# Kernel optimization log

Measured on AMD Instinct MI355X. Metric: run time of the kernel, lower is better.

The kernel has to match this reference:

```python
import jax, jax.numpy as jnp
import numpy as np

B, H, W, C = 32, 56, 56, 256
NH, WS, SH = 8, 7, 3
HD = C // NH
SCALE = HD ** -0.5
N = WS * WS
MLP = 4 * C


def _rel_pos_index():
    coords = np.stack(np.meshgrid(np.arange(WS), np.arange(WS), indexing='ij')).reshape(2, -1)
    rel = (coords[:, :, None] - coords[:, None, :]).transpose(1, 2, 0)
    rel[..., 0] += WS - 1
    rel[..., 1] += WS - 1
    rel[..., 0] *= 2 * WS - 1
    return jnp.asarray(rel.sum(-1))  # (N, N) int


def _attn_mask():
    # standard Swin shifted-window mask, computed statically
    img = np.zeros((H, W))
    cnt = 0
    for hs in (slice(0, -WS), slice(-WS, -SH), slice(-SH, None)):
        for ws_ in (slice(0, -WS), slice(-WS, -SH), slice(-SH, None)):
            img[hs, ws_] = cnt
            cnt += 1
    mw = img.reshape(H // WS, WS, W // WS, WS).transpose(0, 2, 1, 3).reshape(-1, N)
    am = mw[:, None, :] - mw[:, :, None]
    am = np.where(am != 0, -1e9, 0.0).astype(np.float32)
    return jnp.asarray(am)  # (nW, N, N)


def _part(x):
    b = x.shape[0]
    x = x.reshape(b, H // WS, WS, W // WS, WS, C)
    return x.transpose(0, 1, 3, 2, 4, 5).reshape(-1, N, C)


def _rev(xw):
    x = xw.reshape(-1, H // WS, W // WS, WS, WS, C)
    return x.transpose(0, 1, 3, 2, 4, 5).reshape(-1, H, W, C)


def _ln(x, g, b):
    m = x.mean(-1, keepdims=True)
    v = x.var(-1, keepdims=True)
    return (x - m) / jnp.sqrt(v + 1e-5) * g + b


def setup_inputs() -> dict:
    key = jax.random.key(0)
    ks = jax.random.split(key, 6)
    s = 0.02
    return {
        'x': jax.random.normal(ks[0], (B, H, W, C), jnp.float32),
        'gamma1': jnp.ones((C,), jnp.float32),
        'beta1': jnp.zeros((C,), jnp.float32),
        'w_qkv': jax.random.normal(ks[1], (C, 3 * C), jnp.float32) * s,
        'b_qkv': jnp.zeros((3 * C,), jnp.float32),
        'rpb': jax.random.normal(ks[2], ((2 * WS - 1) ** 2, NH), jnp.float32) * s,
        'w_proj': jax.random.normal(ks[3], (C, C), jnp.float32) * s,
        'b_proj': jnp.zeros((C,), jnp.float32),
        'gamma2': jnp.ones((C,), jnp.float32),
        'beta2': jnp.zeros((C,), jnp.float32),
        'w_fc1': jax.random.normal(ks[4], (C, MLP), jnp.float32) * s,
        'b_fc1': jnp.zeros((MLP,), jnp.float32),
        'w_fc2': jax.random.normal(ks[5], (MLP, C), jnp.float32) * s,
        'b_fc2': jnp.zeros((C,), jnp.float32),
    }


def reference(x, gamma1, beta1, w_qkv, b_qkv, rpb, w_proj, b_proj, gamma2, beta2, w_fc1, b_fc1, w_fc2, b_fc2):
    idx = _rel_pos_index()
    mask = _attn_mask()  # (nW, N, N)
    nW = mask.shape[0]

    shortcut = x
    xn = _ln(x, gamma1, beta1)
    xs = jnp.roll(xn, (-SH, -SH), axis=(1, 2))        # cyclic shift
    xw = _part(xs)                                     # (B*nW, N, C)

    qkv = (xw @ w_qkv + b_qkv).reshape(-1, N, 3, NH, HD).transpose(2, 0, 3, 1, 4)
    # SNN-variant IF (ReLU) gates on q, k, v
    q, k, v = jax.nn.relu(qkv[0]), jax.nn.relu(qkv[1]), jax.nn.relu(qkv[2])

    attn = jnp.einsum('bhnd,bhmd->bhnm', q * SCALE, k)  # (B*nW, NH, N, N)
    bias = rpb[idx].transpose(2, 0, 1)                  # (NH, N, N)
    attn = attn + bias[None]
    attn = attn.reshape(-1, nW, NH, N, N) + mask[None, :, None]
    attn = attn.reshape(-1, NH, N, N)
    # stdp_qk ReLU before softmax (faithful to source)
    attn = jax.nn.softmax(jax.nn.relu(attn), axis=-1)
    # stdp_av ReLU on attention output
    out = jax.nn.relu(jnp.einsum('bhnm,bhmd->bhnd', attn, v))
    out = out.transpose(0, 2, 1, 3).reshape(-1, N, C) @ w_proj + b_proj

    xs = _rev(out)
    x = shortcut + jnp.roll(xs, (SH, SH), axis=(1, 2))  # reverse shift + residual

    h = jax.nn.gelu(_ln(x, gamma2, beta2) @ w_fc1 + b_fc1, approximate=False)
    return x + h @ w_fc2 + b_fc2
```

## Files before the change

kernel.cpp:

```cpp
#include <hip/hip_runtime.h>
#include <stdint.h>

typedef unsigned short u16;
typedef short bf16x8 __attribute__((ext_vector_type(8)));
typedef float f32x4 __attribute__((ext_vector_type(4)));

#define NTOK 100352
#define NWIN 2048
#define CC 256
#define NHEAD 8
#define HDIM 32
#define NWT 49
#define MLPD 1024
#define ATT_SCALE 0.17677669529663687f

__device__ __forceinline__ u16 f2b(float f) {
  union { float f; uint32_t u; } c; c.f = f;
  return (u16)((c.u + 0x7fffu + ((c.u >> 16) & 1u)) >> 16);
}
__device__ __forceinline__ float b2f(u16 h) {
  union { uint32_t u; float f; } c; c.u = ((uint32_t)h) << 16;
  return c.f;
}
__device__ __forceinline__ uint32_t f2b2(float lo, float hi) {
  uint32_t r;
  asm("v_cvt_pk_bf16_f32 %0, %1, %2" : "=v"(r) : "v"(lo), "v"(hi));
  return r;
}

__device__ __forceinline__ void gload_lds16(const void* g, void* l) {
  __builtin_amdgcn_global_load_lds((const __attribute__((address_space(1))) void*)g,
                                   (__attribute__((address_space(3))) void*)l, 16, 0, 0);
}

__global__ __launch_bounds__(256)
void prep_k(const float* __restrict__ wqkv, const float* __restrict__ wproj,
            const float* __restrict__ wfc1, const float* __restrict__ wfc2,
            const float* __restrict__ rpb,
            u16* __restrict__ qkvT, u16* __restrict__ projT,
            u16* __restrict__ fc1T, u16* __restrict__ fc2T, float* __restrict__ lut) {
  int i = blockIdx.x * 256 + threadIdx.x;
  if (i < 196608) {
    int k = i / 768, n = i % 768;
    qkvT[(size_t)n * 256 + k] = f2b(wqkv[i]);
  } else if (i < 262144) {
    int j = i - 196608, k = j / 256, n = j % 256;
    projT[(size_t)n * 256 + k] = f2b(wproj[j]);
  } else if (i < 524288) {
    int j = i - 262144, k = j / 1024, n = j % 1024;
    fc1T[(size_t)n * 256 + k] = f2b(wfc1[j]);
  } else if (i < 786432) {
    int j = i - 524288, k = j / 256, n = j % 256;
    fc2T[(size_t)n * 1024 + k] = f2b(wfc2[j]);
  } else if (i < 819200) {
    int j = i - 786432;
    int h = j >> 12, m = (j >> 6) & 63, n = j & 63;
    float v = 0.f;
    if (m < 49 && n < 49) {
      int i1 = n / 7, j1 = n % 7, i2 = m / 7, j2 = m % 7;
      v = rpb[((i1 - i2 + 6) * 13 + (j1 - j2 + 6)) * 8 + h];
    }
    lut[j] = v;
  }
}

__global__ __launch_bounds__(256)
void ln_k(const float* __restrict__ x, const float* __restrict__ g,
          const float* __restrict__ be, u16* __restrict__ out) {
  int token = blockIdx.x * 4 + (threadIdx.x >> 6);
  int lane = threadIdx.x & 63;
  int win = token / 49, nn = token % 49;
  int b = win >> 6, wh = (win >> 3) & 7, ww = win & 7;
  int i = nn / 7, j = nn % 7;
  int h = wh * 7 + i + 3; if (h >= 56) h -= 56;
  int w = ww * 7 + j + 3; if (w >= 56) w -= 56;
  size_t src = ((size_t)((b * 56 + h) * 56 + w)) * CC;
  f32x4 v = *(const f32x4*)&x[src + lane * 4];
  float s1 = v[0] + v[1] + v[2] + v[3];
  float s2 = v[0]*v[0] + v[1]*v[1] + v[2]*v[2] + v[3]*v[3];
#pragma unroll
  for (int o = 32; o; o >>= 1) { s1 += __shfl_xor(s1, o); s2 += __shfl_xor(s2, o); }
  float mean = s1 * (1.f / 256.f);
  float var = s2 * (1.f / 256.f) - mean * mean;
  float rstd = rsqrtf(var + 1e-5f);
  f32x4 gv = *(const f32x4*)&g[lane * 4];
  f32x4 bv = *(const f32x4*)&be[lane * 4];
  float y0 = (v[0]-mean)*rstd*gv[0] + bv[0];
  float y1 = (v[1]-mean)*rstd*gv[1] + bv[1];
  float y2 = (v[2]-mean)*rstd*gv[2] + bv[2];
  float y3 = (v[3]-mean)*rstd*gv[3] + bv[3];
  *(uint2*)&out[(size_t)token * CC + lane * 4] = make_uint2(f2b2(y0, y1), f2b2(y2, y3));
}

#define BM 128
#define BN 128
enum { EPI_QKV = 0 };

template<int EPI, int NKT>
__global__ __launch_bounds__(256)
void gemm_k(const u16* __restrict__ A, const u16* __restrict__ BT,
            const float* __restrict__ bias,
            void* __restrict__ p0, const void* __restrict__ p1) {
  constexpr int K = NKT * 64;
  __shared__ u16 aL[2][BM * 64];
  __shared__ u16 bL[BN * 64];
  const int tid = threadIdx.x;
  const int lane = tid & 63;
  const int wv = tid >> 6;
  const int wm = wv >> 1, wn = wv & 1;

  int bx = blockIdx.x, by = blockIdx.y;
  {
    int nwg = gridDim.x * gridDim.y;
    int lin = by * gridDim.x + bx;
    int q = nwg >> 3, r = nwg & 7;
    int xcd = lin & 7, idx = lin >> 3;
    int wg = (xcd < r ? xcd * (q + 1) : r * (q + 1) + (xcd - r) * q) + idx;
    bx = wg % gridDim.x;
    by = wg / gridDim.x;
  }
  const long m0 = (long)by * BM;
  const int n0 = bx * BN;

  f32x4 acc[4][4] = {};
  const int r15 = lane & 15;
  const int g4 = lane >> 4;

  const u16* pA[4];
  const u16* pB[4];
  int lslot[4];
#pragma unroll
  for (int it = 0; it < 4; ++it) {
    int slot = tid + 256 * it;
    int row = slot >> 3, c8 = slot & 7;
    int cs = c8 ^ (row & 7);
    pA[it] = &A[(m0 + row) * K + cs * 8];
    pB[it] = &BT[(size_t)(n0 + row) * K + cs * 8];
    lslot[it] = slot * 8;
  }
  int aoff[2][4], boff[2][4];
#pragma unroll
  for (int kk = 0; kk < 2; ++kk)
#pragma unroll
    for (int m = 0; m < 4; ++m) {
      int rowa = wm * 64 + m * 16 + r15;
      aoff[kk][m] = rowa * 64 + (((kk * 4 + g4) ^ (rowa & 7)) << 3);
      int rowb = wn * 64 + m * 16 + r15;
      boff[kk][m] = rowb * 64 + (((kk * 4 + g4) ^ (rowb & 7)) << 3);
    }

  auto stageA = [&](int bufi) {
#pragma unroll
    for (int it = 0; it < 4; ++it) { gload_lds16(pA[it], &aL[bufi][lslot[it]]); pA[it] += 64; }
  };
  auto stageB = [&]() {
#pragma unroll
    for (int it = 0; it < 4; ++it) { gload_lds16(pB[it], &bL[lslot[it]]); pB[it] += 64; }
  };

  stageB();
  stageA(0);
  stageA(1);

  for (int t = 0; t < NKT; ++t) {
    if (t + 1 < NKT) asm volatile("s_waitcnt vmcnt(4)" ::: "memory");
    else             asm volatile("s_waitcnt vmcnt(0)" ::: "memory");
    __builtin_amdgcn_sched_barrier(0);
    __builtin_amdgcn_s_barrier();
    __builtin_amdgcn_sched_barrier(0);
    {
      const u16* ab = aL[t & 1];
#pragma unroll
      for (int kk = 0; kk < 2; ++kk) {
        bf16x8 af[4], bfr[4];
#pragma unroll
        for (int m = 0; m < 4; ++m) af[m] = *(const bf16x8*)&ab[aoff[kk][m]];
#pragma unroll
        for (int n = 0; n < 4; ++n) bfr[n] = *(const bf16x8*)&bL[boff[kk][n]];
#pragma unroll
        for (int n = 0; n < 4; ++n)
#pragma unroll
          for (int m = 0; m < 4; ++m)
            acc[n][m] = __builtin_amdgcn_mfma_f32_16x16x32_bf16(bfr[n], af[m], acc[n][m], 0, 0, 0);
      }
    }
    __builtin_amdgcn_sched_barrier(0);
    __builtin_amdgcn_s_barrier();
    __builtin_amdgcn_sched_barrier(0);
    if (t + 1 < NKT) stageB();
    if (t + 2 < NKT) stageA(t & 1);
  }

#pragma unroll
  for (int mt = 0; mt < 4; ++mt) {
    const int mrow = (int)m0 + wm * 64 + mt * 16 + r15;
    int win = mrow / 49, nn = mrow - win * 49;
#pragma unroll
    for (int nt = 0; nt < 4; ++nt) {
      const int col0 = n0 + wn * 64 + nt * 16 + g4 * 4;
      f32x4 bv = *(const f32x4*)&bias[col0];
      f32x4 v;
#pragma unroll
      for (int j = 0; j < 4; ++j) v[j] = acc[nt][mt][j] + bv[j];
      int s = col0 >> 8, head = (col0 >> 5) & 7, d0 = col0 & 31;
      float sc = (s == 0) ? ATT_SCALE : 1.f;
#pragma unroll
      for (int j = 0; j < 4; ++j) v[j] = fmaxf(v[j], 0.f) * sc;
      u16* dst = (u16*)p0 + (size_t)s * ((size_t)NTOK * CC);
      *(uint2*)&dst[(((size_t)(win * NHEAD + head)) * NWT + nn) * HDIM + d0] =
          make_uint2(f2b2(v[0], v[1]), f2b2(v[2], v[3]));
    }
  }
}

__global__ __launch_bounds__(512)
void gemm_ln_k(const u16* __restrict__ A, const u16* __restrict__ BT,
               const float* __restrict__ bias, const float* __restrict__ xres,
               const float* __restrict__ g2, const float* __restrict__ be2,
               u16* __restrict__ x2, u16* __restrict__ xn2) {
  constexpr int K = 256;
  constexpr int NKT = 4;
  __shared__ u16 aL[2][128 * 64];
  __shared__ u16 bL[256 * 64];
  __shared__ float st[4 * 128 * 2];
  const int tid = threadIdx.x;
  const int lane = tid & 63;
  const int wv = tid >> 6;
  const int wm = wv >> 2;
  const int wn = wv & 3;
  const int r15 = lane & 15;
  const int g4 = lane >> 4;

  int by = blockIdx.x;
  {
    int nwg = gridDim.x;
    int q = nwg >> 3, r = nwg & 7;
    int xcd = by & 7, idx = by >> 3;
    by = (xcd < r ? xcd * (q + 1) : r * (q + 1) + (xcd - r) * q) + idx;
  }
  const long m0 = (long)by * 128;

  f32x4 acc[4][4] = {};

  const u16* pA[2];
  int la[2];
#pragma unroll
  for (int it = 0; it < 2; ++it) {
    int slot = tid + 512 * it;
    int row = slot >> 3, c8 = slot & 7;
    int cs = c8 ^ (row & 7);
    pA[it] = &A[(m0 + row) * K + cs * 8];
    la[it] = slot * 8;
  }
  const u16* pB[4];
  int lb[4];
#pragma unroll
  for (int it = 0; it < 4; ++it) {
    int slot = tid + 512 * it;
    int row = slot >> 3, c8 = slot & 7;
    int cs = c8 ^ (row & 7);
    pB[it] = &BT[(size_t)row * K + cs * 8];
    lb[it] = slot * 8;
  }
  int aoff[2][4], boff[2][4];
#pragma unroll
  for (int kk = 0; kk < 2; ++kk)
#pragma unroll
    for (int m = 0; m < 4; ++m) {
      int rowa = wm * 64 + m * 16 + r15;
      aoff[kk][m] = rowa * 64 + (((kk * 4 + g4) ^ (rowa & 7)) << 3);
      int rowb = wn * 64 + m * 16 + r15;
      boff[kk][m] = rowb * 64 + (((kk * 4 + g4) ^ (rowb & 7)) << 3);
    }

  auto stageA = [&](int bufi) {
#pragma unroll
    for (int it = 0; it < 2; ++it) { gload_lds16(pA[it], &aL[bufi][la[it]]); pA[it] += 64; }
  };
  auto stageB = [&]() {
#pragma unroll
    for (int it = 0; it < 4; ++it) { gload_lds16(pB[it], &bL[lb[it]]); pB[it] += 64; }
  };

  stageB();
  stageA(0);
  stageA(1);

  for (int t = 0; t < NKT; ++t) {
    if (t + 1 < NKT) asm volatile("s_waitcnt vmcnt(2)" ::: "memory");
    else             asm volatile("s_waitcnt vmcnt(0)" ::: "memory");
    __builtin_amdgcn_sched_barrier(0);
    __builtin_amdgcn_s_barrier();
    __builtin_amdgcn_sched_barrier(0);
    {
      const u16* ab = aL[t & 1];
#pragma unroll
      for (int kk = 0; kk < 2; ++kk) {
        bf16x8 af[4], bfr[4];
#pragma unroll
        for (int m = 0; m < 4; ++m) af[m] = *(const bf16x8*)&ab[aoff[kk][m]];
#pragma unroll
        for (int n = 0; n < 4; ++n) bfr[n] = *(const bf16x8*)&bL[boff[kk][n]];
#pragma unroll
        for (int n = 0; n < 4; ++n)
#pragma unroll
          for (int m = 0; m < 4; ++m)
            acc[n][m] = __builtin_amdgcn_mfma_f32_16x16x32_bf16(bfr[n], af[m], acc[n][m], 0, 0, 0);
      }
    }
    __builtin_amdgcn_sched_barrier(0);
    __builtin_amdgcn_s_barrier();
    __builtin_amdgcn_sched_barrier(0);
    if (t + 1 < NKT) stageB();
    if (t + 2 < NKT) stageA(t & 1);
  }

  size_t pix[4];
  float s1[4] = {}, s2[4] = {};
#pragma unroll
  for (int mt = 0; mt < 4; ++mt) {
    const int mrow = (int)m0 + wm * 64 + mt * 16 + r15;
    int win = mrow / 49, nn = mrow - win * 49;
    int b = win >> 6, wh = (win >> 3) & 7, ww = win & 7;
    int i = nn / 7, jj = nn - i * 7;
    int h = wh * 7 + i + 3; if (h >= 56) h -= 56;
    int w = ww * 7 + jj + 3; if (w >= 56) w -= 56;
    pix[mt] = (size_t)((b * 56 + h) * 56 + w);
#pragma unroll
    for (int nt = 0; nt < 4; ++nt) {
      const int col0 = wn * 64 + nt * 16 + g4 * 4;
      f32x4 bv = *(const f32x4*)&bias[col0];
      f32x4 r = *(const f32x4*)&xres[pix[mt] * CC + col0];
      f32x4 v;
#pragma unroll
      for (int j = 0; j < 4; ++j) {
        v[j] = acc[nt][mt][j] + bv[j] + r[j];
        s1[mt] += v[j];
        s2[mt] += v[j] * v[j];
      }
      *(uint2*)&x2[(size_t)mrow * CC + col0] =
          make_uint2(f2b2(v[0], v[1]), f2b2(v[2], v[3]));
      acc[nt][mt] = v;
    }
    s1[mt] += __shfl_xor(s1[mt], 16);  s1[mt] += __shfl_xor(s1[mt], 32);
    s2[mt] += __shfl_xor(s2[mt], 16);  s2[mt] += __shfl_xor(s2[mt], 32);
    if (g4 == 0) {
      int wrow = wm * 64 + mt * 16 + r15;
      st[(wn * 128 + wrow) * 2 + 0] = s1[mt];
      st[(wn * 128 + wrow) * 2 + 1] = s2[mt];
    }
  }
  __syncthreads();
#pragma unroll
  for (int mt = 0; mt < 4; ++mt) {
    const int mrow = (int)m0 + wm * 64 + mt * 16 + r15;
    int wrow = wm * 64 + mt * 16 + r15;
    float t1 = 0.f, t2 = 0.f;
#pragma unroll
    for (int w2 = 0; w2 < 4; ++w2) {
      t1 += st[(w2 * 128 + wrow) * 2 + 0];
      t2 += st[(w2 * 128 + wrow) * 2 + 1];
    }
    float mean = t1 * (1.f / 256.f);
    float var = t2 * (1.f / 256.f) - mean * mean;
    float rstd = rsqrtf(var + 1e-5f);
#pragma unroll
    for (int nt = 0; nt < 4; ++nt) {
      const int col0 = wn * 64 + nt * 16 + g4 * 4;
      f32x4 gv = *(const f32x4*)&g2[col0];
      f32x4 bv = *(const f32x4*)&be2[col0];
      float y0 = (acc[nt][mt][0] - mean) * rstd * gv[0] + bv[0];
      float y1 = (acc[nt][mt][1] - mean) * rstd * gv[1] + bv[1];
      float y2 = (acc[nt][mt][2] - mean) * rstd * gv[2] + bv[2];
      float y3 = (acc[nt][mt][3] - mean) * rstd * gv[3] + bv[3];
      *(uint2*)&xn2[(size_t)mrow * CC + col0] = make_uint2(f2b2(y0, y1), f2b2(y2, y3));
    }
  }
}

__global__ __launch_bounds__(512, 4)
void mlp_fused_k(const u16* __restrict__ xn, const u16* __restrict__ fc1T,
                 const u16* __restrict__ fc2T, const float* __restrict__ b1,
                 const float* __restrict__ b2v, const u16* __restrict__ x2,
                 float* __restrict__ outp) {
  __shared__ u16 lds[24576];
  u16* shA0 = lds;
  u16* shA1 = lds + 4096;
  u16* shB1 = lds + 8192;
  u16* shB2 = lds;
  u16* shH  = lds + 16384;

  const int tid = threadIdx.x;
  const int lane = tid & 63;
  const int wv = tid >> 6;
  const int wmw = wv >> 2;
  const int wnw = wv & 3;
  const int r15 = lane & 15;
  const int g4 = lane >> 4;

  int by = blockIdx.x;
  {
    int nwg = gridDim.x;
    int q = nwg >> 3, r = nwg & 7;
    int xcd = by & 7, idx = by >> 3;
    by = (xcd < r ? xcd * (q + 1) : r * (q + 1) + (xcd - r) * q) + idx;
  }
  const long m0 = (long)by * 64;

  const int rowA = tid >> 3, csA = (tid & 7) ^ (rowA & 7);
  const u16* pAbase = &xn[(m0 + rowA) * 256 + csA * 8];
  int rowB1[2], lb1[2];
  const u16* pB1base[2];
#pragma unroll
  for (int it = 0; it < 2; ++it) {
    int slot = tid + 512 * it;
    rowB1[it] = slot >> 3;
    int cs = (slot & 7) ^ (rowB1[it] & 7);
    pB1base[it] = &fc1T[(size_t)rowB1[it] * 256 + cs * 8];
    lb1[it] = slot * 8;
  }
  int lb2[4];
  const u16* pB2base[4];
#pragma unroll
  for (int it = 0; it < 4; ++it) {
    int slot = tid + 512 * it;
    int row = slot >> 3;
    int cs = (slot & 7) ^ (row & 7);
    pB2base[it] = &fc2T[(size_t)row * 1024 + cs * 8];
    lb2[it] = slot * 8;
  }

  int a1off[2][2], b1off[2][2];
#pragma unroll
  for (int kk = 0; kk < 2; ++kk)
#pragma unroll
    for (int m = 0; m < 2; ++m) {
      int ra = wmw * 32 + m * 16 + r15;
      a1off[kk][m] = ra * 64 + (((kk * 4 + g4) ^ (ra & 7)) << 3);
      int rb = wnw * 32 + m * 16 + r15;
      b1off[kk][m] = rb * 64 + (((kk * 4 + g4) ^ (rb & 7)) << 3);
    }
  int b2off[2][4];
#pragma unroll
  for (int kk = 0; kk < 2; ++kk)
#pragma unroll
    for (int n = 0; n < 4; ++n) {
      int rb = wnw * 64 + n * 16 + r15;
      b2off[kk][n] = rb * 64 + (((kk * 4 + g4) ^ (rb & 7)) << 3);
    }

  f32x4 oacc[4][2] = {};

  for (int hc = 0; hc < 8; ++hc) {
    const size_t b1chunk = (size_t)hc * 128 * 256;
    gload_lds16(pB1base[0] + b1chunk, &shB1[lb1[0]]);
    gload_lds16(pB1base[1] + b1chunk, &shB1[lb1[1]]);
    gload_lds16(pAbase,      &shA0[tid * 8]);
    gload_lds16(pAbase + 64, &shA1[tid * 8]);

    f32x4 acc1[2][2] = {};
    for (int t = 0; t < 4; ++t) {
      if (t + 1 < 4) asm volatile("s_waitcnt vmcnt(1)" ::: "memory");
      else           asm volatile("s_waitcnt vmcnt(0)" ::: "memory");
      __builtin_amdgcn_sched_barrier(0);
      __builtin_amdgcn_s_barrier();
      __builtin_amdgcn_sched_barrier(0);
      {
        const u16* ab = (t & 1) ? shA1 : shA0;
#pragma unroll
        for (int kk = 0; kk < 2; ++kk) {
          bf16x8 af[2], bfr[2];
#pragma unroll
          for (int m = 0; m < 2; ++m) af[m] = *(const bf16x8*)&ab[a1off[kk][m]];
#pragma unroll
          for (int n = 0; n < 2; ++n) bfr[n] = *(const bf16x8*)&shB1[b1off[kk][n]];
#pragma unroll
          for (int n = 0; n < 2; ++n)
#pragma unroll
            for (int m = 0; m < 2; ++m)
              acc1[n][m] = __builtin_amdgcn_mfma_f32_16x16x32_bf16(bfr[n], af[m], acc1[n][m], 0, 0, 0);
        }
      }
      __builtin_amdgcn_sched_barrier(0);
      __builtin_amdgcn_s_barrier();
      __builtin_amdgcn_sched_barrier(0);
      if (t + 1 < 4) {
        gload_lds16(pB1base[0] + b1chunk + (t + 1) * 64, &shB1[lb1[0]]);
        gload_lds16(pB1base[1] + b1chunk + (t + 1) * 64, &shB1[lb1[1]]);
      }
      if (t + 2 < 4) {
        u16* dst = (t & 1) ? shA1 : shA0;
        gload_lds16(pAbase + (t + 2) * 64, &dst[tid * 8]);
      }
    }
    gload_lds16(pB2base[0] + hc * 128, &shB2[lb2[0]]);
    gload_lds16(pB2base[1] + hc * 128, &shB2[lb2[1]]);
    gload_lds16(pB2base[2] + hc * 128, &shB2[lb2[2]]);
    gload_lds16(pB2base[3] + hc * 128, &shB2[lb2[3]]);

#pragma unroll
    for (int mt = 0; mt < 2; ++mt) {
      const int hrow = wmw * 32 + mt * 16 + r15;
#pragma unroll
      for (int nt = 0; nt < 2; ++nt) {
        const int col0 = wnw * 32 + nt * 16 + g4 * 4;
        f32x4 bv = *(const f32x4*)&b1[hc * 128 + col0];
        f32x4 v;
#pragma unroll
        for (int j = 0; j < 4; ++j) {
          float u = acc1[nt][mt][j] + bv[j];
          float u2 = u * u;
          float tt = u * fmaf(0.044715f, u2, 1.f);
          float e = exp2f(tt * -2.3022029f);
          v[j] = u * __builtin_amdgcn_rcpf(1.f + e);
        }
        int hidx = hrow * 128 + (((col0 >> 3) ^ (hrow & 15)) << 3) + (col0 & 4);
        *(uint2*)&shH[hidx] = make_uint2(f2b2(v[0], v[1]), f2b2(v[2], v[3]));
      }
    }
    asm volatile("s_waitcnt lgkmcnt(0)" ::: "memory");
    __builtin_amdgcn_sched_barrier(0);
    asm volatile("s_waitcnt vmcnt(0)" ::: "memory");
    __builtin_amdgcn_sched_barrier(0);
    __builtin_amdgcn_s_barrier();
    __builtin_amdgcn_sched_barrier(0);

#pragma unroll
    for (int kt = 0; kt < 2; ++kt) {
#pragma unroll
      for (int kk = 0; kk < 2; ++kk) {
        bf16x8 af[2], bfr[4];
#pragma unroll
        for (int m = 0; m < 2; ++m) {
          int hrow = wmw * 32 + m * 16 + r15;
          int kchunk = kt * 8 + kk * 4 + g4;
          af[m] = *(const bf16x8*)&shH[hrow * 128 + ((kchunk ^ (hrow & 15)) << 3)];
        }
#pragma unroll
        for (int n = 0; n < 4; ++n) bfr[n] = *(const bf16x8*)&shB2[b2off[kk][n]];
#pragma unroll
        for (int n = 0; n < 4; ++n)
#pragma unroll
          for (int m = 0; m < 2; ++m)
            oacc[n][m] = __builtin_amdgcn_mfma_f32_16x16x32_bf16(bfr[n], af[m], oacc[n][m], 0, 0, 0);
      }
      __builtin_amdgcn_sched_barrier(0);
      __builtin_amdgcn_s_barrier();
      __builtin_amdgcn_sched_barrier(0);
      if (kt == 0) {
        gload_lds16(pB2base[0] + hc * 128 + 64, &shB2[lb2[0]]);
        gload_lds16(pB2base[1] + hc * 128 + 64, &shB2[lb2[1]]);
        gload_lds16(pB2base[2] + hc * 128 + 64, &shB2[lb2[2]]);
        gload_lds16(pB2base[3] + hc * 128 + 64, &shB2[lb2[3]]);
        asm volatile("s_waitcnt vmcnt(0)" ::: "memory");
        __builtin_amdgcn_sched_barrier(0);
        __builtin_amdgcn_s_barrier();
        __builtin_amdgcn_sched_barrier(0);
      }
    }
  }

#pragma unroll
  for (int mt = 0; mt < 2; ++mt) {
    const int mrow = (int)m0 + wmw * 32 + mt * 16 + r15;
    int win = mrow / 49, nn = mrow - win * 49;
    int b = win >> 6, wh = (win >> 3) & 7, ww = win & 7;
    int i = nn / 7, jj = nn - i * 7;
    int h = wh * 7 + i + 3; if (h >= 56) h -= 56;
    int w = ww * 7 + jj + 3; if (w >= 56) w -= 56;
    size_t pix = (size_t)((b * 56 + h) * 56 + w);
#pragma unroll
    for (int nt = 0; nt < 4; ++nt) {
      const int col0 = wnw * 64 + nt * 16 + g4 * 4;
      f32x4 bv = *(const f32x4*)&b2v[col0];
      f32x4 v;
#pragma unroll
      for (int j = 0; j < 4; ++j) v[j] = oacc[nt][mt][j] + bv[j];
      uint2 rb = *(const uint2*)&x2[(size_t)mrow * CC + col0];
      v[0] += b2f((u16)(rb.x & 0xffffu));
      v[1] += b2f((u16)(rb.x >> 16));
      v[2] += b2f((u16)(rb.y & 0xffffu));
      v[3] += b2f((u16)(rb.y >> 16));
      *(f32x4*)&outp[pix * CC + col0] = v;
    }
  }
}

__global__ __launch_bounds__(256)
void attn_mfma_k(const u16* __restrict__ q, const u16* __restrict__ k2,
                 const u16* __restrict__ v2, const float* __restrict__ lut,
                 u16* __restrict__ out) {
  __shared__ u16 P_lds[4][64 * 72];
  const int tid = threadIdx.x;
  const int wv = tid >> 6;
  const int lane = tid & 63;
  const int c = lane & 15;
  const int g = lane >> 4;
  const int blk = blockIdx.x * 4 + wv;
  const int head = blk & 7;
  const int win = blk >> 3;
  const int wimg = win & 63;
  const int wh = wimg >> 3, ww = wimg & 7;
  const size_t base = (size_t)blk * (NWT * HDIM);
  u16* Pw = P_lds[wv];

  bf16x8 kf[4], qf[4];
#pragma unroll
  for (int t = 0; t < 4; ++t) {
    kf[t] = *(const bf16x8*)&k2[base + (size_t)(t * 16 + c) * HDIM + g * 8];
    qf[t] = *(const bf16x8*)&q [base + (size_t)(t * 16 + c) * HDIM + g * 8];
  }
  bf16x8 vf[2][2];
#pragma unroll
  for (int kcc = 0; kcc < 2; ++kcc)
#pragma unroll
    for (int td = 0; td < 2; ++td)
#pragma unroll
      for (int jj = 0; jj < 8; ++jj) {
        int m = kcc * 32 + g * 8 + jj;
        m = m < 49 ? m : 48;
        vf[kcc][td][jj] = (short)v2[base + (size_t)m * HDIM + td * 16 + c];
      }

  f32x4 acc[4][4] = {};
#pragma unroll
  for (int tm = 0; tm < 4; ++tm)
#pragma unroll
    for (int tn = 0; tn < 4; ++tn)
      acc[tm][tn] = __builtin_amdgcn_mfma_f32_16x16x32_bf16(kf[tm], qf[tn], acc[tm][tn], 0, 0, 0);

  const float* lrow = &lut[(size_t)head * 64 * 64];
  int Ln[4];
#pragma unroll
  for (int tn = 0; tn < 4; ++tn) {
    int n = tn * 16 + c;
    int i1 = (n * 9363) >> 16;
    int j1 = n - i1 * 7;
    int rh = (wh < 7) ? 0 : (i1 < 4 ? 1 : 2);
    int rw = (ww < 7) ? 0 : (j1 < 4 ? 1 : 2);
    Ln[tn] = rh * 3 + rw;
  }
  float colmax[4] = {0.f, 0.f, 0.f, 0.f};
#pragma unroll
  for (int tm = 0; tm < 4; ++tm)
#pragma unroll
    for (int j = 0; j < 4; ++j) {
      int m = tm * 16 + g * 4 + j;
      int i2 = (m * 9363) >> 16;
      int j2 = m - i2 * 7;
      int rh = (wh < 7) ? 0 : (i2 < 4 ? 1 : 2);
      int rw = (ww < 7) ? 0 : (j2 < 4 ? 1 : 2);
      int Lm = rh * 3 + rw;
#pragma unroll
      for (int tn = 0; tn < 4; ++tn) {
        float s = acc[tm][tn][j] + lrow[m * 64 + tn * 16 + c];
        s = fmaxf(s, 0.f);
        if (Lm != Ln[tn]) s = 0.f;
        acc[tm][tn][j] = s;
        colmax[tn] = fmaxf(colmax[tn], s);
      }
    }
#pragma unroll
  for (int tn = 0; tn < 4; ++tn) {
    colmax[tn] = fmaxf(colmax[tn], __shfl_xor(colmax[tn], 16));
    colmax[tn] = fmaxf(colmax[tn], __shfl_xor(colmax[tn], 32));
  }
  float colsum[4] = {0.f, 0.f, 0.f, 0.f};
#pragma unroll
  for (int tm = 0; tm < 4; ++tm)
#pragma unroll
    for (int j = 0; j < 4; ++j) {
      int m = tm * 16 + g * 4 + j;
      bool mvalid = (m < NWT);
#pragma unroll
      for (int tn = 0; tn < 4; ++tn) {
        float e = mvalid ? __expf(acc[tm][tn][j] - colmax[tn]) : 0.f;
        acc[tm][tn][j] = e;
        colsum[tn] += e;
      }
    }
#pragma unroll
  for (int tn = 0; tn < 4; ++tn) {
    colsum[tn] += __shfl_xor(colsum[tn], 16);
    colsum[tn] += __shfl_xor(colsum[tn], 32);
    colsum[tn] = 1.f / colsum[tn];
  }

#pragma unroll
  for (int tn = 0; tn < 4; ++tn) {
    int n = tn * 16 + c;
#pragma unroll
    for (int tm = 0; tm < 4; ++tm) {
      float r = colsum[tn];
      *(uint2*)&Pw[n * 72 + tm * 16 + g * 4] =
          make_uint2(f2b2(acc[tm][tn][0] * r, acc[tm][tn][1] * r),
                     f2b2(acc[tm][tn][2] * r, acc[tm][tn][3] * r));
    }
  }

  f32x4 oacc[4][2] = {};
#pragma unroll
  for (int kcc = 0; kcc < 2; ++kcc) {
    bf16x8 pf[4];
#pragma unroll
    for (int tr = 0; tr < 4; ++tr)
      pf[tr] = *(const bf16x8*)&Pw[(tr * 16 + c) * 72 + kcc * 32 + g * 8];
#pragma unroll
    for (int tr = 0; tr < 4; ++tr)
#pragma unroll
      for (int td = 0; td < 2; ++td)
        oacc[tr][td] = __builtin_amdgcn_mfma_f32_16x16x32_bf16(pf[tr], vf[kcc][td], oacc[tr][td], 0, 0, 0);
  }

#pragma unroll
  for (int tr = 0; tr < 4; ++tr)
#pragma unroll
    for (int j = 0; j < 4; ++j) {
      int n = tr * 16 + g * 4 + j;
      if (n < NWT) {
#pragma unroll
        for (int td = 0; td < 2; ++td) {
          int d = td * 16 + c;
          out[((size_t)(win * NWT + n)) * CC + head * HDIM + d] =
              f2b(fmaxf(oacc[tr][td][j], 0.f));
        }
      }
    }
}

extern "C" void kernel_launch(void* const* d_in, const int* in_sizes, int n_in,
                              void* d_out, int out_size, void* d_ws, size_t ws_size,
                              hipStream_t stream) {
  const float* x      = (const float*)d_in[0];
  const float* gamma1 = (const float*)d_in[1];
  const float* beta1  = (const float*)d_in[2];
  const float* w_qkv  = (const float*)d_in[3];
  const float* b_qkv  = (const float*)d_in[4];
  const float* rpb    = (const float*)d_in[5];
  const float* w_proj = (const float*)d_in[6];
  const float* b_proj = (const float*)d_in[7];
  const float* gamma2 = (const float*)d_in[8];
  const float* beta2  = (const float*)d_in[9];
  const float* w_fc1  = (const float*)d_in[10];
  const float* b_fc1  = (const float*)d_in[11];
  const float* w_fc2  = (const float*)d_in[12];
  const float* b_fc2  = (const float*)d_in[13];
  float* out = (float*)d_out;

  char* ws = (char*)d_ws;
  size_t off = 0;
  auto alloc = [&](size_t bytes) { void* p = ws + off; off = (off + bytes + 255) & ~(size_t)255; return p; };

  u16* wqkvT = (u16*)alloc(768 * 256 * 2);
  u16* wprojT = (u16*)alloc(256 * 256 * 2);
  u16* wfc1T = (u16*)alloc(1024 * 256 * 2);
  u16* wfc2T = (u16*)alloc(256 * 1024 * 2);
  float* lut = (float*)alloc(8 * 64 * 64 * 4);
  u16* region2 = (u16*)alloc((size_t)NTOK * CC * 2);
  char* region1 = (char*)alloc((size_t)3 * NTOK * CC * 2);

  u16* xw = region2;
  u16* qb = (u16*)region1;
  u16* kb = qb + (size_t)NTOK * CC;
  u16* vb = kb + (size_t)NTOK * CC;
  u16* attn_out = region2;
  u16* x2 = (u16*)region1;
  u16* xn2 = x2 + (size_t)NTOK * CC;

  if (ws_size < off) return;

  prep_k<<<3200, 256, 0, stream>>>(w_qkv, w_proj, w_fc1, w_fc2, rpb,
                                   wqkvT, wprojT, wfc1T, wfc2T, lut);

  ln_k<<<NTOK / 4, 256, 0, stream>>>(x, gamma1, beta1, xw);

  gemm_k<EPI_QKV, 4><<<dim3(768 / BN, NTOK / BM), 256, 0, stream>>>(
      xw, wqkvT, b_qkv, (void*)qb, nullptr);

  attn_mfma_k<<<NWIN * NHEAD / 4, 256, 0, stream>>>(qb, kb, vb, lut, attn_out);

  gemm_ln_k<<<NTOK / 128, 512, 0, stream>>>(
      attn_out, wprojT, b_proj, x, gamma2, beta2, x2, xn2);

  mlp_fused_k<<<NTOK / 64, 512, 0, stream>>>(
      xn2, wfc1T, wfc2T, b_fc1, b_fc2, x2, out);
}
```

Baseline: 459.3 us.

## Widen MLP fc1 K-tile to 128 and double-buffer fc2 weight tiles

In the fused MLP kernel, the fc1 stage now loads 128-wide K slices of activations and weights, so each hidden chunk takes two pipeline steps instead of four. The swizzle changes from 8 to 16 chunks per row to match. Both halves of the fc2 weight slice are fetched into separate LDS buffers at once, which removes one barrier and the serialized reload of the second half. The cost is LDS growing from 48 KB to 80 KB per block, which can cut the number of resident blocks per CU and reduce latency hiding.

Measured after the change: 435.9 us. 1.05x faster.

```diff
diff --git a/kernel.cpp b/kernel.cpp
--- a/kernel.cpp
+++ b/kernel.cpp
@@ -383,12 +383,13 @@
                  const u16* __restrict__ fc2T, const float* __restrict__ b1,
                  const float* __restrict__ b2v, const u16* __restrict__ x2,
                  float* __restrict__ outp) {
-  __shared__ u16 lds[24576];
+  __shared__ u16 lds[40960];
   u16* shA0 = lds;
-  u16* shA1 = lds + 4096;
-  u16* shB1 = lds + 8192;
-  u16* shB2 = lds;
-  u16* shH  = lds + 16384;
+  u16* shA1 = lds + 8192;
+  u16* shB1 = lds + 16384;
+  u16* shB2_0 = lds;
+  u16* shB2_1 = lds + 16384;
+  u16* shH  = lds + 32768;
 
   const int tid = threadIdx.x;
   const int lane = tid & 63;
@@ -407,16 +408,24 @@
   }
   const long m0 = (long)by * 64;
 
-  const int rowA = tid >> 3, csA = (tid & 7) ^ (rowA & 7);
-  const u16* pAbase = &xn[(m0 + rowA) * 256 + csA * 8];
-  int rowB1[2], lb1[2];
-  const u16* pB1base[2];
+  int laA[2];
+  const u16* pAbase[2];
 #pragma unroll
   for (int it = 0; it < 2; ++it) {
     int slot = tid + 512 * it;
-    rowB1[it] = slot >> 3;
-    int cs = (slot & 7) ^ (rowB1[it] & 7);
-    pB1base[it] = &fc1T[(size_t)rowB1[it] * 256 + cs * 8];
+    int row = slot >> 4, c16 = slot & 15;
+    int cs = c16 ^ (row & 15);
+    pAbase[it] = &xn[(m0 + row) * 256 + cs * 8];
+    laA[it] = slot * 8;
+  }
+  int lb1[4];
+  const u16* pB1base[4];
+#pragma unroll
+  for (int it = 0; it < 4; ++it) {
+    int slot = tid + 512 * it;
+    int row = slot >> 4, c16 = slot & 15;
+    int cs = c16 ^ (row & 15);
+    pB1base[it] = &fc1T[(size_t)row * 256 + cs * 8];
     lb1[it] = slot * 8;
   }
   int lb2[4];
@@ -424,21 +433,21 @@
 #pragma unroll
   for (int it = 0; it < 4; ++it) {
     int slot = tid + 512 * it;
-    int row = slot >> 3;
-    int cs = (slot & 7) ^ (row & 7);
+    int row = slot >> 3, c8 = slot & 7;
+    int cs = c8 ^ (row & 7);
     pB2base[it] = &fc2T[(size_t)row * 1024 + cs * 8];
     lb2[it] = slot * 8;
   }
 
-  int a1off[2][2], b1off[2][2];
-#pragma unroll
-  for (int kk = 0; kk < 2; ++kk)
+  int a1off[4][2], b1off[4][2];
+#pragma unroll
+  for (int kk = 0; kk < 4; ++kk)
 #pragma unroll
     for (int m = 0; m < 2; ++m) {
       int ra = wmw * 32 + m * 16 + r15;
-      a1off[kk][m] = ra * 64 + (((kk * 4 + g4) ^ (ra & 7)) << 3);
+      a1off[kk][m] = ra * 128 + (((kk * 4 + g4) ^ (ra & 15)) << 3);
       int rb = wnw * 32 + m * 16 + r15;
-      b1off[kk][m] = rb * 64 + (((kk * 4 + g4) ^ (rb & 7)) << 3);
+      b1off[kk][m] = rb * 128 + (((kk * 4 + g4) ^ (rb & 15)) << 3);
     }
   int b2off[2][4];
 #pragma unroll
@@ -455,20 +464,25 @@
     const size_t b1chunk = (size_t)hc * 128 * 256;
     gload_lds16(pB1base[0] + b1chunk, &shB1[lb1[0]]);
     gload_lds16(pB1base[1] + b1chunk, &shB1[lb1[1]]);
-    gload_lds16(pAbase,      &shA0[tid * 8]);
-    gload_lds16(pAbase + 64, &shA1[tid * 8]);
+    gload_lds16(pB1base[2] + b1chunk, &shB1[lb1[2]]);
+    gload_lds16(pB1base[3] + b1chunk, &shB1[lb1[3]]);
+    gload_lds16(pAbase[0],       &shA0[laA[0]]);
+    gload_lds16(pAbase[1],       &shA0[laA[1]]);
+    gload_lds16(pAbase[0] + 128, &shA1[laA[0]]);
+    gload_lds16(pAbase[1] + 128, &shA1[laA[1]]);
 
     f32x4 acc1[2][2] = {};
-    for (int t = 0; t < 4; ++t) {
-      if (t + 1 < 4) asm volatile("s_waitcnt vmcnt(1)" ::: "memory");
-      else           asm volatile("s_waitcnt vmcnt(0)" ::: "memory");
+#pragma unroll
+    for (int t = 0; t < 2; ++t) {
+      if (t == 0) asm volatile("s_waitcnt vmcnt(2)" ::: "memory");
+      else        asm volatile("s_waitcnt vmcnt(0)" ::: "memory");
       __builtin_amdgcn_sched_barrier(0);
       __builtin_amdgcn_s_barrier();
       __builtin_amdgcn_sched_barrier(0);
       {
-        const u16* ab = (t & 1) ? shA1 : shA0;
-#pragma unroll
-        for (int kk = 0; kk < 2; ++kk) {
+        const u16* ab = t ? shA1 : shA0;
+#pragma unroll
+        for (int kk = 0; kk < 4; ++kk) {
           bf16x8 af[2], bfr[2];
 #pragma unroll
           for (int m = 0; m < 2; ++m) af[m] = *(const bf16x8*)&ab[a1off[kk][m]];
@@ -484,19 +498,21 @@
       __builtin_amdgcn_sched_barrier(0);
       __builtin_amdgcn_s_barrier();
       __builtin_amdgcn_sched_barrier(0);
-      if (t + 1 < 4) {
-        gload_lds16(pB1base[0] + b1chunk + (t + 1) * 64, &shB1[lb1[0]]);
-        gload_lds16(pB1base[1] + b1chunk + (t + 1) * 64, &shB1[lb1[1]]);
-      }
-      if (t + 2 < 4) {
-        u16* dst = (t & 1) ? shA1 : shA0;
-        gload_lds16(pAbase + (t + 2) * 64, &dst[tid * 8]);
-      }
-    }
-    gload_lds16(pB2base[0] + hc * 128, &shB2[lb2[0]]);
-    gload_lds16(pB2base[1] + hc * 128, &shB2[lb2[1]]);
-    gload_lds16(pB2base[2] + hc * 128, &shB2[lb2[2]]);
-    gload_lds16(pB2base[3] + hc * 128, &shB2[lb2[3]]);
+      if (t == 0) {
+        gload_lds16(pB1base[0] + b1chunk + 128, &shB1[lb1[0]]);
+        gload_lds16(pB1base[1] + b1chunk + 128, &shB1[lb1[1]]);
+        gload_lds16(pB1base[2] + b1chunk + 128, &shB1[lb1[2]]);
+        gload_lds16(pB1base[3] + b1chunk + 128, &shB1[lb1[3]]);
+      }
+    }
+    gload_lds16(pB2base[0] + hc * 128, &shB2_0[lb2[0]]);
+    gload_lds16(pB2base[1] + hc * 128, &shB2_0[lb2[1]]);
+    gload_lds16(pB2base[2] + hc * 128, &shB2_0[lb2[2]]);
+    gload_lds16(pB2base[3] + hc * 128, &shB2_0[lb2[3]]);
+    gload_lds16(pB2base[0] + hc * 128 + 64, &shB2_1[lb2[0]]);
+    gload_lds16(pB2base[1] + hc * 128 + 64, &shB2_1[lb2[1]]);
+    gload_lds16(pB2base[2] + hc * 128 + 64, &shB2_1[lb2[2]]);
+    gload_lds16(pB2base[3] + hc * 128 + 64, &shB2_1[lb2[3]]);
 
 #pragma unroll
     for (int mt = 0; mt < 2; ++mt) {
@@ -514,19 +530,20 @@
           float e = exp2f(tt * -2.3022029f);
           v[j] = u * __builtin_amdgcn_rcpf(1.f + e);
         }
-        int hidx = hrow * 128 + (((col0 >> 3) ^ (hrow & 15)) << 3) + (col0 & 4);
+        int hidx = hrow * 128 + (((col0 >> 3) ^ (hrow & 15)) << 3) + (col0 & 7);
         *(uint2*)&shH[hidx] = make_uint2(f2b2(v[0], v[1]), f2b2(v[2], v[3]));
       }
     }
     asm volatile("s_waitcnt lgkmcnt(0)" ::: "memory");
     __builtin_amdgcn_sched_barrier(0);
-    asm volatile("s_waitcnt vmcnt(0)" ::: "memory");
+    asm volatile("s_waitcnt vmcnt(4)" ::: "memory");
     __builtin_amdgcn_sched_barrier(0);
     __builtin_amdgcn_s_barrier();
     __builtin_amdgcn_sched_barrier(0);
 
 #pragma unroll
     for (int kt = 0; kt < 2; ++kt) {
+      const u16* bb = kt ? shB2_1 : shB2_0;
 #pragma unroll
       for (int kk = 0; kk < 2; ++kk) {
         bf16x8 af[2], bfr[4];
@@ -537,22 +554,19 @@
           af[m] = *(const bf16x8*)&shH[hrow * 128 + ((kchunk ^ (hrow & 15)) << 3)];
         }
 #pragma unroll
-        for (int n = 0; n < 4; ++n) bfr[n] = *(const bf16x8*)&shB2[b2off[kk][n]];
+        for (int n = 0; n < 4; ++n) bfr[n] = *(const bf16x8*)&bb[b2off[kk][n]];
 #pragma unroll
         for (int n = 0; n < 4; ++n)
 #pragma unroll
           for (int m = 0; m < 2; ++m)
             oacc[n][m] = __builtin_amdgcn_mfma_f32_16x16x32_bf16(bfr[n], af[m], oacc[n][m], 0, 0, 0);
       }
-      __builtin_amdgcn_sched_barrier(0);
-      __builtin_amdgcn_s_barrier();
-      __builtin_amdgcn_sched_barrier(0);
       if (kt == 0) {
-        gload_lds16(pB2base[0] + hc * 128 + 64, &shB2[lb2[0]]);
-        gload_lds16(pB2base[1] + hc * 128 + 64, &shB2[lb2[1]]);
-        gload_lds16(pB2base[2] + hc * 128 + 64, &shB2[lb2[2]]);
-        gload_lds16(pB2base[3] + hc * 128 + 64, &shB2[lb2[3]]);
         asm volatile("s_waitcnt vmcnt(0)" ::: "memory");
+        __builtin_amdgcn_sched_barrier(0);
+        __builtin_amdgcn_s_barrier();
+        __builtin_amdgcn_sched_barrier(0);
+      } else {
         __builtin_amdgcn_sched_barrier(0);
         __builtin_amdgcn_s_barrier();
         __builtin_amdgcn_sched_barrier(0);
```
